# Performance work log

Hardware: AMD Instinct MI355X
Metric: run time of the kernel (lower is better)

Reference implementation:

```python
import jax, jax.numpy as jnp
import numpy as np

N = 50000
E = 800000
F_IN = 128
F_HID = 256   # 2 * out_channels
F_OUT = 128


def setup_inputs() -> dict:
    key = jax.random.key(0)
    ks = jax.random.split(key, 6)
    x = jax.random.normal(ks[0], (N, F_IN), dtype=jnp.float32)
    edge_index = jax.random.randint(ks[1], (2, E), 0, N, dtype=jnp.int64)
    # GCNConv params: glorot weight + zero bias (PyG default)
    s1 = (6.0 / (F_IN + F_HID)) ** 0.5
    s2 = (6.0 / (F_HID + F_OUT)) ** 0.5
    W1 = jax.random.uniform(ks[2], (F_IN, F_HID), jnp.float32, -s1, s1)
    b1 = jnp.zeros((F_HID,), jnp.float32)
    W2 = jax.random.uniform(ks[3], (F_HID, F_OUT), jnp.float32, -s2, s2)
    b2 = jnp.zeros((F_OUT,), jnp.float32)
    return {"x": x, "edge_index": edge_index, "W1": W1, "b1": b1, "W2": W2, "b2": b2}


def _gcn_conv(x, W, b, src, dst, deg_inv_sqrt, n):
    # norm per edge (self-loops already appended to src/dst)
    norm = deg_inv_sqrt[src] * deg_inv_sqrt[dst]          # [E+N]
    h = x @ W                                             # [N, F_out]
    msg = h[src] * norm[:, None]                          # [E+N, F_out] gather
    out = jax.ops.segment_sum(msg, dst, num_segments=n)   # scatter-add
    return out + b


def reference(x, edge_index, W1, b1, W2, b2):
    n = x.shape[0]
    loops = jnp.arange(n, dtype=edge_index.dtype)
    src = jnp.concatenate([edge_index[0], loops])
    dst = jnp.concatenate([edge_index[1], loops])
    # symmetric normalization with self-loops (PyG GCNConv default)
    deg = jax.ops.segment_sum(jnp.ones_like(dst, dtype=x.dtype), dst, num_segments=n)
    deg_inv_sqrt = jnp.where(deg > 0, jax.lax.rsqrt(jnp.maximum(deg, 1e-12)), 0.0)
    h = jax.nn.relu(_gcn_conv(x, W1, b1, src, dst, deg_inv_sqrt, n))
    h = jax.nn.relu(_gcn_conv(h, W2, b2, src, dst, deg_inv_sqrt, n))
    return h
```

## Files before the change

### kernel.cpp

```cpp
#include <hip/hip_runtime.h>


typedef short bf16x8 __attribute__((ext_vector_type(8)));
typedef float f32x4 __attribute__((ext_vector_type(4)));

#define LDSTRIDE 264
#define XTSTRIDE 136
#define BSHIFT 7
#define BMASK 127

__device__ inline unsigned short f2bf(float f) {
    unsigned int u = __float_as_uint(f);
    u += 0x7FFF + ((u >> 16) & 1);
    return (unsigned short)(u >> 16);
}
__device__ inline float bf2f(unsigned short h) {
    return __uint_as_float(((unsigned int)h) << 16);
}

__device__ inline void swz1(const float* W, unsigned short* Ws, int K, int N, int i) {
    int k = i / N, n = i % N;
    int KC = K >> 5;
    size_t d = ((((size_t)(n >> 4) * KC + (k >> 5)) * 64) + ((k >> 3) & 3) * 16 + (n & 15)) * 8
               + (k & 7);
    Ws[d] = f2bf(W[i]);
}
__global__ void wswz_kernel(const float* __restrict__ W1, const float* __restrict__ W2,
                            unsigned short* __restrict__ W1s, unsigned short* __restrict__ W2s,
                            int* __restrict__ ctrl) {
    int i = blockIdx.x * blockDim.x + threadIdx.x;
    if (blockIdx.x == 0) {
        for (int j = threadIdx.x; j < 512; j += 256) ctrl[j] = 0;
    }
    if (i < 32768) swz1(W1, W1s, 128, 256, i);
    else if (i < 65536) swz1(W2, W2s, 256, 128, i - 32768);
}

__global__ __launch_bounds__(256) void bin_kernel(
    const int* __restrict__ src, const int* __restrict__ dst,
    int* __restrict__ bcur, unsigned int* __restrict__ bbuf,
    int E, int cap, int nbuck) {
    __shared__ int cnt[512];
    __shared__ int base[512];
    int t = threadIdx.x;
    for (int i = t; i < nbuck; i += 256) cnt[i] = 0;
    __syncthreads();
    int e0 = blockIdx.x * 2048;
    unsigned int p_[8];
    int b_[8];
#pragma unroll
    for (int i = 0; i < 8; i++) {
        int e = e0 + i * 256 + t;
        if (e < E) {
            int s = src[e], d = dst[e];
            b_[i] = d >> BSHIFT;
            p_[i] = ((unsigned)(d & BMASK) << 24) | (unsigned)s;
            atomicAdd(&cnt[b_[i]], 1);
        } else b_[i] = -1;
    }
    __syncthreads();
    for (int b = t; b < nbuck; b += 256) {
        int c = cnt[b];
        base[b] = (c > 0) ? atomicAdd(&bcur[b], c) : 0;
    }
    __syncthreads();
    for (int i = t; i < nbuck; i += 256) cnt[i] = 0;
    __syncthreads();
#pragma unroll
    for (int i = 0; i < 8; i++) {
        if (b_[i] >= 0) {
            int b = b_[i];
            int p = base[b] + atomicAdd(&cnt[b], 1);
            if (p >= 0 && p < cap) bbuf[(size_t)b * cap + p] = p_[i];
        }
    }
}

__global__ __launch_bounds__(256) void bucket_csr_kernel(
    const int* __restrict__ bcur, const unsigned int* __restrict__ bbuf,
    const float* __restrict__ x,
    int* __restrict__ col, int* __restrict__ rowbeg, int* __restrict__ rowend,
    float* __restrict__ dinv, unsigned short* __restrict__ Xs, int N, int cap) {
    __shared__ int ldeg[128];
    __shared__ int lrp[256];
    __shared__ float sdv[128];
    int b = blockIdx.x, t = threadIdx.x;
    int cnt = min(max(bcur[b], 0), cap);
    if (t < 128) ldeg[t] = 0;
    __syncthreads();
    const unsigned int* mybuf = bbuf + (size_t)b * cap;
    for (int i = t; i < cnt; i += 256)
        atomicAdd(&ldeg[mybuf[i] >> 24], 1);
    __syncthreads();
    int v = (t < 128) ? ldeg[t] : 0;
    lrp[t] = v;
    __syncthreads();
    for (int off = 1; off < 128; off <<= 1) {
        int u = (t >= off) ? lrp[t - off] : 0;
        __syncthreads();
        lrp[t] += u;
        __syncthreads();
    }
    int excl = lrp[t] - v;
    int gbase = b * cap;
    if (t < 128) {
        int r = b * 128 + t;
        float dv = rsqrtf((float)v + 1.0f);
        sdv[t] = dv;
        if (r < N) {
            rowbeg[r] = gbase + excl;
            rowend[r] = gbase + excl + v;
            dinv[r] = dv;
        }
        ldeg[t] = excl;
    }
    __syncthreads();
    for (int i = t; i < cnt; i += 256) {
        unsigned int pr = mybuf[i];
        int p = atomicAdd(&ldeg[pr >> 24], 1);
        col[gbase + p] = (int)(pr & 0xffffffu);
    }
    int rbase = b * 128;
    for (int i = t; i < 128 * 32; i += 256) {
        int rl = i >> 5;
        int gr = rbase + rl;
        if (gr >= N) break;
        float s = sdv[rl];
        float4 xv = ((const float4*)x)[(size_t)gr * 32 + (i & 31)];
        ushort4 o;
        o.x = f2bf(xv.x * s); o.y = f2bf(xv.y * s);
        o.z = f2bf(xv.z * s); o.w = f2bf(xv.w * s);
        ((ushort4*)Xs)[(size_t)gr * 32 + (i & 31)] = o;
    }
}

__global__ __launch_bounds__(256) void gather2_kernel(
    const int* __restrict__ rowbeg, const int* __restrict__ rowend,
    const int* __restrict__ col, const unsigned short* __restrict__ P,
    const float* __restrict__ dinv, const float* __restrict__ bias,
    float* __restrict__ OF, int N) {
    int gid = blockIdx.x * blockDim.x + threadIdx.x;
    int r = gid >> 5;
    if (r >= N) return;
    int lane = gid & 31;
    const size_t off = (size_t)lane * 4;
    const unsigned short* Pf = P + off;

    ushort4 u = *(const ushort4*)(Pf + (size_t)r * 128);
    float ax = bf2f(u.x), ay = bf2f(u.y), az = bf2f(u.z), aw = bf2f(u.w);

    int beg = rowbeg[r], end = rowend[r];
    int i = beg;
    for (; i + 7 < end; i += 8) {
        ushort4 v0 = *(const ushort4*)(Pf + (size_t)col[i + 0] * 128);
        ushort4 v1 = *(const ushort4*)(Pf + (size_t)col[i + 1] * 128);
        ushort4 v2 = *(const ushort4*)(Pf + (size_t)col[i + 2] * 128);
        ushort4 v3 = *(const ushort4*)(Pf + (size_t)col[i + 3] * 128);
        ushort4 v4 = *(const ushort4*)(Pf + (size_t)col[i + 4] * 128);
        ushort4 v5 = *(const ushort4*)(Pf + (size_t)col[i + 5] * 128);
        ushort4 v6 = *(const ushort4*)(Pf + (size_t)col[i + 6] * 128);
        ushort4 v7 = *(const ushort4*)(Pf + (size_t)col[i + 7] * 128);
        ax += bf2f(v0.x) + bf2f(v1.x) + bf2f(v2.x) + bf2f(v3.x)
            + bf2f(v4.x) + bf2f(v5.x) + bf2f(v6.x) + bf2f(v7.x);
        ay += bf2f(v0.y) + bf2f(v1.y) + bf2f(v2.y) + bf2f(v3.y)
            + bf2f(v4.y) + bf2f(v5.y) + bf2f(v6.y) + bf2f(v7.y);
        az += bf2f(v0.z) + bf2f(v1.z) + bf2f(v2.z) + bf2f(v3.z)
            + bf2f(v4.z) + bf2f(v5.z) + bf2f(v6.z) + bf2f(v7.z);
        aw += bf2f(v0.w) + bf2f(v1.w) + bf2f(v2.w) + bf2f(v3.w)
            + bf2f(v4.w) + bf2f(v5.w) + bf2f(v6.w) + bf2f(v7.w);
    }
    for (; i < end; i++) {
        ushort4 a = *(const ushort4*)(Pf + (size_t)col[i] * 128);
        ax += bf2f(a.x); ay += bf2f(a.y); az += bf2f(a.z); aw += bf2f(a.w);
    }
    float s = dinv[r];
    float4 bb = *(const float4*)(bias + off);
    float4 o;
    o.x = fmaxf(ax * s + bb.x, 0.f);
    o.y = fmaxf(ay * s + bb.y, 0.f);
    o.z = fmaxf(az * s + bb.z, 0.f);
    o.w = fmaxf(aw * s + bb.w, 0.f);
    *(float4*)(OF + (size_t)r * 128 + off) = o;
}

__global__ __launch_bounds__(256, 4) void gemm_fused_kernel(
    const int* __restrict__ rowbeg, const int* __restrict__ rowend,
    const int* __restrict__ col, const unsigned short* __restrict__ Xs,
    const unsigned short* __restrict__ W1s, const unsigned short* __restrict__ W2s,
    const float* __restrict__ bias, const float* __restrict__ dinv,
    unsigned short* __restrict__ T, int M) {
    __shared__ unsigned short Xt[16 * XTSTRIDE];
    __shared__ unsigned short Ht[16 * LDSTRIDE];

    int t = threadIdx.x;
    int m0 = blockIdx.x * 16;
    int hw = t >> 5;
    int l  = t & 31;
    const unsigned short* Pf = Xs + (size_t)l * 4;

#pragma unroll
    for (int sub = 0; sub < 2; sub++) {
        int lr = hw * 2 + sub;
        int r = m0 + lr;
        int rc = (r < M) ? r : (M - 1);
        ushort4 u = *(const ushort4*)(Pf + (size_t)rc * 128);
        float ax = bf2f(u.x), ay = bf2f(u.y), az = bf2f(u.z), aw = bf2f(u.w);
        int beg = rowbeg[rc], end = rowend[rc];
        int i = beg;
        for (; i + 7 < end; i += 8) {
            ushort4 v0 = *(const ushort4*)(Pf + (size_t)col[i + 0] * 128);
            ushort4 v1 = *(const ushort4*)(Pf + (size_t)col[i + 1] * 128);
            ushort4 v2 = *(const ushort4*)(Pf + (size_t)col[i + 2] * 128);
            ushort4 v3 = *(const ushort4*)(Pf + (size_t)col[i + 3] * 128);
            ushort4 v4 = *(const ushort4*)(Pf + (size_t)col[i + 4] * 128);
            ushort4 v5 = *(const ushort4*)(Pf + (size_t)col[i + 5] * 128);
            ushort4 v6 = *(const ushort4*)(Pf + (size_t)col[i + 6] * 128);
            ushort4 v7 = *(const ushort4*)(Pf + (size_t)col[i + 7] * 128);
            ax += bf2f(v0.x) + bf2f(v1.x) + bf2f(v2.x) + bf2f(v3.x)
                + bf2f(v4.x) + bf2f(v5.x) + bf2f(v6.x) + bf2f(v7.x);
            ay += bf2f(v0.y) + bf2f(v1.y) + bf2f(v2.y) + bf2f(v3.y)
                + bf2f(v4.y) + bf2f(v5.y) + bf2f(v6.y) + bf2f(v7.y);
            az += bf2f(v0.z) + bf2f(v1.z) + bf2f(v2.z) + bf2f(v3.z)
                + bf2f(v4.z) + bf2f(v5.z) + bf2f(v6.z) + bf2f(v7.z);
            aw += bf2f(v0.w) + bf2f(v1.w) + bf2f(v2.w) + bf2f(v3.w)
                + bf2f(v4.w) + bf2f(v5.w) + bf2f(v6.w) + bf2f(v7.w);
        }
        for (; i < end; i++) {
            ushort4 a = *(const ushort4*)(Pf + (size_t)col[i] * 128);
            ax += bf2f(a.x); ay += bf2f(a.y); az += bf2f(a.z); aw += bf2f(a.w);
        }
        float dvr = dinv[rc];
        ushort4 o;
        o.x = f2bf(ax * dvr); o.y = f2bf(ay * dvr);
        o.z = f2bf(az * dvr); o.w = f2bf(aw * dvr);
        *(ushort4*)(Xt + lr * XTSTRIDE + l * 4) = o;
    }
    __syncthreads();

    int wave = t >> 6;
    int lane = t & 63;
    int mrow = lane & 15, quad = lane >> 4;

    bf16x8 a[4];
#pragma unroll
    for (int kc = 0; kc < 4; kc++)
        a[kc] = *(const bf16x8*)(Xt + mrow * XTSTRIDE + kc * 32 + quad * 8);

    float dv[4];
#pragma unroll
    for (int i2 = 0; i2 < 4; i2++) {
        int gr = m0 + quad * 4 + i2;
        dv[i2] = dinv[gr < M ? gr : M - 1];
    }

    const bf16x8* w1v = (const bf16x8*)W1s;
    for (int nt = wave * 4; nt < wave * 4 + 4; nt++) {
        f32x4 c = {0.f, 0.f, 0.f, 0.f};
#pragma unroll
        for (int kc = 0; kc < 4; kc++) {
            bf16x8 b = w1v[(nt * 4 + kc) * 64 + lane];
            c = __builtin_amdgcn_mfma_f32_16x16x32_bf16(a[kc], b, c, 0, 0, 0);
        }
        int colc = nt * 16 + mrow;
        float bb = bias[colc];
#pragma unroll
        for (int i2 = 0; i2 < 4; i2++) {
            float v = fmaxf(c[i2] + bb, 0.f) * dv[i2];
            Ht[(quad * 4 + i2) * LDSTRIDE + colc] = f2bf(v);
        }
    }
    __syncthreads();

    bf16x8 hh[8];
    const unsigned short* hrow = Ht + mrow * LDSTRIDE + quad * 8;
#pragma unroll
    for (int kc = 0; kc < 8; kc++) hh[kc] = *(const bf16x8*)(hrow + kc * 32);
    const bf16x8* w2v = (const bf16x8*)W2s;
    for (int nt = wave * 2; nt < wave * 2 + 2; nt++) {
        f32x4 c = {0.f, 0.f, 0.f, 0.f};
#pragma unroll
        for (int kc = 0; kc < 8; kc++) {
            bf16x8 b = w2v[(nt * 8 + kc) * 64 + lane];
            c = __builtin_amdgcn_mfma_f32_16x16x32_bf16(hh[kc], b, c, 0, 0, 0);
        }
        int colc = nt * 16 + mrow;
#pragma unroll
        for (int i2 = 0; i2 < 4; i2++) {
            int gr = m0 + quad * 4 + i2;
            if (gr < M) T[(size_t)gr * 128 + colc] = f2bf(c[i2]);
        }
    }
}

extern "C" void kernel_launch(void* const* d_in, const int* in_sizes, int n_in,
                              void* d_out, int out_size, void* d_ws, size_t ws_size,
                              hipStream_t stream) {
    const float* x  = (const float*)d_in[0];
    const int* ei   = (const int*)d_in[1];
    const float* W1 = (const float*)d_in[2];
    const float* b1 = (const float*)d_in[3];
    const float* W2 = (const float*)d_in[4];
    const float* b2 = (const float*)d_in[5];
    float* out      = (float*)d_out;

    const int N = in_sizes[0] / 128;
    const int E = in_sizes[1] / 2;
    const int* src = ei;
    const int* dst = ei + E;

    const int nbuck = (N + BMASK) >> BSHIFT;
    const int cap = E / nbuck + E / (4 * nbuck) + 512;

    float* ws = (float*)d_ws;
    size_t Np = ((size_t)N + 255) & ~(size_t)255;
    float*          dinv = ws;
    unsigned short* Ts   = (unsigned short*)(dinv + Np);
    unsigned short* Xs   = Ts + (size_t)N * 128;
    unsigned short* W1s  = Xs + (size_t)N * 128;
    unsigned short* W2s  = W1s + 32768;
    int* rowbeg = (int*)(W2s + 32768);
    int* rowend = rowbeg + Np;
    int* ctrl   = rowend + Np;
    int* bcur   = ctrl;
    unsigned int* bbuf = (unsigned int*)(ctrl + 512);
    int* col    = (int*)(bbuf + (size_t)nbuck * cap);

    wswz_kernel<<<256, 256, 0, stream>>>(W1, W2, W1s, W2s, ctrl);
    int nbins = (E + 2047) / 2048;
    bin_kernel<<<nbins, 256, 0, stream>>>(src, dst, bcur, bbuf, E, cap, nbuck);
    bucket_csr_kernel<<<nbuck, 256, 0, stream>>>(bcur, bbuf, x, col, rowbeg, rowend,
                                                 dinv, Xs, N, cap);

    int mtiles = (N + 15) / 16;
    gemm_fused_kernel<<<mtiles, 256, 0, stream>>>(rowbeg, rowend, col, Xs,
                                                  W1s, W2s, b1, dinv, Ts, N);

    int gth = N * 32;
    gather2_kernel<<<(gth + 255) / 256, 256, 0, stream>>>(rowbeg, rowend, col, Ts,
                                                          dinv, b2, out, N);
}
```

Before: 199.4 us.

## Double fused GEMM block to 512 threads and predicate gather tail loads

The fused gather+GEMM kernel now launches 512 threads per 16-row tile. Each half-wave aggregates one row instead of two, and each wave computes half as many MFMA column tiles, which exposes more parallelism for the latency-bound neighbour gather. In both gather loops the scalar remainder loop is replaced by one masked 8-wide batch that clamps indices and multiplies by 0/1 masks, so the tail loads can be issued together. The cost is extra redundant loads and multiplies on short tails, plus possible lower occupancy or register pressure at the larger block size.

```diff
diff --git a/kernel.cpp b/kernel.cpp
--- a/kernel.cpp
+++ b/kernel.cpp
@@ -169,9 +169,32 @@
         aw += bf2f(v0.w) + bf2f(v1.w) + bf2f(v2.w) + bf2f(v3.w)
             + bf2f(v4.w) + bf2f(v5.w) + bf2f(v6.w) + bf2f(v7.w);
     }
-    for (; i < end; i++) {
-        ushort4 a = *(const ushort4*)(Pf + (size_t)col[i] * 128);
-        ax += bf2f(a.x); ay += bf2f(a.y); az += bf2f(a.z); aw += bf2f(a.w);
+    if (i < end) {
+        int cl = end - 1;
+        int e1 = i + 1 < end ? i + 1 : cl, e2 = i + 2 < end ? i + 2 : cl;
+        int e3 = i + 3 < end ? i + 3 : cl, e4 = i + 4 < end ? i + 4 : cl;
+        int e5 = i + 5 < end ? i + 5 : cl, e6 = i + 6 < end ? i + 6 : cl;
+        int e7 = i + 7 < end ? i + 7 : cl;
+        float m1 = i + 1 < end ? 1.f : 0.f, m2 = i + 2 < end ? 1.f : 0.f;
+        float m3 = i + 3 < end ? 1.f : 0.f, m4 = i + 4 < end ? 1.f : 0.f;
+        float m5 = i + 5 < end ? 1.f : 0.f, m6 = i + 6 < end ? 1.f : 0.f;
+        float m7 = i + 7 < end ? 1.f : 0.f;
+        ushort4 v0 = *(const ushort4*)(Pf + (size_t)col[i] * 128);
+        ushort4 v1 = *(const ushort4*)(Pf + (size_t)col[e1] * 128);
+        ushort4 v2 = *(const ushort4*)(Pf + (size_t)col[e2] * 128);
+        ushort4 v3 = *(const ushort4*)(Pf + (size_t)col[e3] * 128);
+        ushort4 v4 = *(const ushort4*)(Pf + (size_t)col[e4] * 128);
+        ushort4 v5 = *(const ushort4*)(Pf + (size_t)col[e5] * 128);
+        ushort4 v6 = *(const ushort4*)(Pf + (size_t)col[e6] * 128);
+        ushort4 v7 = *(const ushort4*)(Pf + (size_t)col[e7] * 128);
+        ax += bf2f(v0.x) + m1 * bf2f(v1.x) + m2 * bf2f(v2.x) + m3 * bf2f(v3.x)
+            + m4 * bf2f(v4.x) + m5 * bf2f(v5.x) + m6 * bf2f(v6.x) + m7 * bf2f(v7.x);
+        ay += bf2f(v0.y) + m1 * bf2f(v1.y) + m2 * bf2f(v2.y) + m3 * bf2f(v3.y)
+            + m4 * bf2f(v4.y) + m5 * bf2f(v5.y) + m6 * bf2f(v6.y) + m7 * bf2f(v7.y);
+        az += bf2f(v0.z) + m1 * bf2f(v1.z) + m2 * bf2f(v2.z) + m3 * bf2f(v3.z)
+            + m4 * bf2f(v4.z) + m5 * bf2f(v5.z) + m6 * bf2f(v6.z) + m7 * bf2f(v7.z);
+        aw += bf2f(v0.w) + m1 * bf2f(v1.w) + m2 * bf2f(v2.w) + m3 * bf2f(v3.w)
+            + m4 * bf2f(v4.w) + m5 * bf2f(v5.w) + m6 * bf2f(v6.w) + m7 * bf2f(v7.w);
     }
     float s = dinv[r];
     float4 bb = *(const float4*)(bias + off);
@@ -183,7 +206,7 @@
     *(float4*)(OF + (size_t)r * 128 + off) = o;
 }
 
-__global__ __launch_bounds__(256, 4) void gemm_fused_kernel(
+__global__ __launch_bounds__(512, 4) void gemm_fused_kernel(
     const int* __restrict__ rowbeg, const int* __restrict__ rowend,
     const int* __restrict__ col, const unsigned short* __restrict__ Xs,
     const unsigned short* __restrict__ W1s, const unsigned short* __restrict__ W2s,
@@ -198,10 +221,8 @@
     int l  = t & 31;
     const unsigned short* Pf = Xs + (size_t)l * 4;
 
-#pragma unroll
-    for (int sub = 0; sub < 2; sub++) {
-        int lr = hw * 2 + sub;
-        int r = m0 + lr;
+    {
+        int r = m0 + hw;
         int rc = (r < M) ? r : (M - 1);
         ushort4 u = *(const ushort4*)(Pf + (size_t)rc * 128);
         float ax = bf2f(u.x), ay = bf2f(u.y), az = bf2f(u.z), aw = bf2f(u.w);
@@ -225,15 +246,38 @@
             aw += bf2f(v0.w) + bf2f(v1.w) + bf2f(v2.w) + bf2f(v3.w)
                 + bf2f(v4.w) + bf2f(v5.w) + bf2f(v6.w) + bf2f(v7.w);
         }
-        for (; i < end; i++) {
-            ushort4 a = *(const ushort4*)(Pf + (size_t)col[i] * 128);
-            ax += bf2f(a.x); ay += bf2f(a.y); az += bf2f(a.z); aw += bf2f(a.w);
+        if (i < end) {
+            int cl = end - 1;
+            int e1 = i + 1 < end ? i + 1 : cl, e2 = i + 2 < end ? i + 2 : cl;
+            int e3 = i + 3 < end ? i + 3 : cl, e4 = i + 4 < end ? i + 4 : cl;
+            int e5 = i + 5 < end ? i + 5 : cl, e6 = i + 6 < end ? i + 6 : cl;
+            int e7 = i + 7 < end ? i + 7 : cl;
+            float m1 = i + 1 < end ? 1.f : 0.f, m2 = i + 2 < end ? 1.f : 0.f;
+            float m3 = i + 3 < end ? 1.f : 0.f, m4 = i + 4 < end ? 1.f : 0.f;
+            float m5 = i + 5 < end ? 1.f : 0.f, m6 = i + 6 < end ? 1.f : 0.f;
+            float m7 = i + 7 < end ? 1.f : 0.f;
+            ushort4 v0 = *(const ushort4*)(Pf + (size_t)col[i] * 128);
+            ushort4 v1 = *(const ushort4*)(Pf + (size_t)col[e1] * 128);
+            ushort4 v2 = *(const ushort4*)(Pf + (size_t)col[e2] * 128);
+            ushort4 v3 = *(const ushort4*)(Pf + (size_t)col[e3] * 128);
+            ushort4 v4 = *(const ushort4*)(Pf + (size_t)col[e4] * 128);
+            ushort4 v5 = *(const ushort4*)(Pf + (size_t)col[e5] * 128);
+            ushort4 v6 = *(const ushort4*)(Pf + (size_t)col[e6] * 128);
+            ushort4 v7 = *(const ushort4*)(Pf + (size_t)col[e7] * 128);
+            ax += bf2f(v0.x) + m1 * bf2f(v1.x) + m2 * bf2f(v2.x) + m3 * bf2f(v3.x)
+                + m4 * bf2f(v4.x) + m5 * bf2f(v5.x) + m6 * bf2f(v6.x) + m7 * bf2f(v7.x);
+            ay += bf2f(v0.y) + m1 * bf2f(v1.y) + m2 * bf2f(v2.y) + m3 * bf2f(v3.y)
+                + m4 * bf2f(v4.y) + m5 * bf2f(v5.y) + m6 * bf2f(v6.y) + m7 * bf2f(v7.y);
+            az += bf2f(v0.z) + m1 * bf2f(v1.z) + m2 * bf2f(v2.z) + m3 * bf2f(v3.z)
+                + m4 * bf2f(v4.z) + m5 * bf2f(v5.z) + m6 * bf2f(v6.z) + m7 * bf2f(v7.z);
+            aw += bf2f(v0.w) + m1 * bf2f(v1.w) + m2 * bf2f(v2.w) + m3 * bf2f(v3.w)
+                + m4 * bf2f(v4.w) + m5 * bf2f(v5.w) + m6 * bf2f(v6.w) + m7 * bf2f(v7.w);
         }
         float dvr = dinv[rc];
         ushort4 o;
         o.x = f2bf(ax * dvr); o.y = f2bf(ay * dvr);
         o.z = f2bf(az * dvr); o.w = f2bf(aw * dvr);
-        *(ushort4*)(Xt + lr * XTSTRIDE + l * 4) = o;
+        *(ushort4*)(Xt + hw * XTSTRIDE + l * 4) = o;
     }
     __syncthreads();
 
@@ -254,7 +298,7 @@
     }
 
     const bf16x8* w1v = (const bf16x8*)W1s;
-    for (int nt = wave * 4; nt < wave * 4 + 4; nt++) {
+    for (int nt = wave * 2; nt < wave * 2 + 2; nt++) {
         f32x4 c = {0.f, 0.f, 0.f, 0.f};
 #pragma unroll
         for (int kc = 0; kc < 4; kc++) {
@@ -276,7 +320,8 @@
 #pragma unroll
     for (int kc = 0; kc < 8; kc++) hh[kc] = *(const bf16x8*)(hrow + kc * 32);
     const bf16x8* w2v = (const bf16x8*)W2s;
-    for (int nt = wave * 2; nt < wave * 2 + 2; nt++) {
+    {
+        int nt = wave;
         f32x4 c = {0.f, 0.f, 0.f, 0.f};
 #pragma unroll
         for (int kc = 0; kc < 8; kc++) {
@@ -332,7 +377,7 @@
                                                  dinv, Xs, N, cap);
 
     int mtiles = (N + 15) / 16;
-    gemm_fused_kernel<<<mtiles, 256, 0, stream>>>(rowbeg, rowend, col, Xs,
+    gemm_fused_kernel<<<mtiles, 512, 0, stream>>>(rowbeg, rowend, col, Xs,
                                                   W1s, W2s, b1, dinv, Ts, N);
 
     int gth = N * 32;
```

Measured after the change: 192.7 us. -3.4%, faster.
